# Optimization experiments

Hardware: AMD Instinct MI355X
Metric: run time of the kernel (lower is better)

Reference implementation:

```python
import jax, jax.numpy as jnp
import numpy as np

SEQ_LEN = 4096
EMBED = 1024
HIDDEN = 128
BATCH = 8


def setup_inputs() -> dict:
    key = jax.random.key(0)
    k_in, k_q, k_k, k_v = jax.random.split(key, 4)
    inputs = jax.random.normal(k_in, (BATCH, SEQ_LEN, EMBED), dtype=jnp.float32)
    # nn.Linear(embed, hidden, bias=False) weights; stored [hidden, embed] in torch,
    # we keep [embed, hidden] for x @ W.
    scale = 1.0 / np.sqrt(EMBED)
    Wq = jax.random.uniform(k_q, (EMBED, HIDDEN), jnp.float32, -scale, scale)
    Wk = jax.random.uniform(k_k, (EMBED, HIDDEN), jnp.float32, -scale, scale)
    Wv = jax.random.uniform(k_v, (EMBED, HIDDEN), jnp.float32, -scale, scale)
    return {"inputs": inputs, "Wq": Wq, "Wk": Wk, "Wv": Wv}


def reference(inputs, Wq, Wk, Wv):
    # Single-head causal scaled dot-product attention.
    q = jnp.einsum("bse,eh->bsh", inputs, Wq)
    k = jnp.einsum("bse,eh->bsh", inputs, Wk)
    v = jnp.einsum("bse,eh->bsh", inputs, Wv)
    d_k = q.shape[-1]
    q = q / jnp.sqrt(jnp.asarray(d_k, q.dtype))
    scores = jnp.einsum("bqh,bkh->bqk", q, k)  # [B, S, S]
    seq = scores.shape[-1]
    causal = jnp.tril(jnp.ones((seq, seq), dtype=bool))
    scores = jnp.where(causal, scores, jnp.asarray(-jnp.inf, scores.dtype))
    weights = jax.nn.softmax(scores, axis=-1)
    return jnp.einsum("bqk,bkh->bqh", weights, v)
```

## Files before the change

### kernel.cpp

```cpp
#include <hip/hip_runtime.h>
#include <stdint.h>

#define B_ 8
#define S_ 4096
#define E_ 1024
#define H_ 128
#define M_ (B_*S_)

typedef __attribute__((ext_vector_type(8))) short short8;
typedef __attribute__((ext_vector_type(4))) float f32x4;
typedef __attribute__((ext_vector_type(16))) float f32x16;

static constexpr float QSCALE = 0.08838834764831845f;

__device__ __forceinline__ unsigned short f2bf(float f) {
    uint32_t u = __float_as_uint(f);
    u += 0x7fffu + ((u >> 16) & 1u);
    return (unsigned short)(u >> 16);
}

__device__ __forceinline__ uint32_t cvt_pk_bf16(float a, float b) {
    uint32_t r;
    asm("v_cvt_pk_bf16_f32 %0, %1, %2" : "=v"(r) : "v"(a), "v"(b));
    return r;
}

__device__ __forceinline__ void gl16(const void* g, void* s) {
    __builtin_amdgcn_global_load_lds(
        (const __attribute__((address_space(1))) unsigned int*)g,
        (__attribute__((address_space(3))) unsigned int*)s, 16, 0, 0);
}

__global__ __launch_bounds__(256)
void prep_w_kernel(const float* __restrict__ Wq, const float* __restrict__ Wk,
                   const float* __restrict__ Wv, unsigned short* __restrict__ Wt)
{
    int id = blockIdx.x*256 + threadIdx.x;
    int which = id >> 14;
    int rem = id & 16383;
    int h = rem >> 7, kc = rem & 127;
    const float* __restrict__ W = (which==0)?Wq:((which==1)?Wk:Wv);
    const float scale = (which==0)? QSCALE : 1.0f;
    uint32_t u[4];
    #pragma unroll
    for (int p=0;p<4;++p) {
        unsigned short a = f2bf(W[(size_t)(kc*8 + 2*p  )*H_ + h] * scale);
        unsigned short b = f2bf(W[(size_t)(kc*8 + 2*p+1)*H_ + h] * scale);
        u[p] = (uint32_t)a | ((uint32_t)b << 16);
    }
    uint4 v; v.x=u[0]; v.y=u[1]; v.z=u[2]; v.w=u[3];
    *(uint4*)(Wt + (size_t)(which*H_ + h)*E_ + kc*8) = v;
}

__global__ __launch_bounds__(512)
void proj_kernel(const float* __restrict__ x, const unsigned short* __restrict__ Wt,
                 unsigned short* __restrict__ Qg, unsigned short* __restrict__ Kg,
                 unsigned short* __restrict__ Vtg)
{
    const int t = threadIdx.x;
    const int w = t >> 6, l = t & 63;
    const int grp = l >> 4, li = l & 15;
    const int rg = w & 3, cg = w >> 2;
    const int rb = blockIdx.x;
    const int row0 = rb * 128;

    __shared__ __align__(128) unsigned char smem[65536];
    unsigned char* sX = smem;
    unsigned char* sW = smem + 16384;
    unsigned short* epi = (unsigned short*)smem;

    f32x4 acc[2][12];
    const f32x4 zz = {0.f,0.f,0.f,0.f};
    #pragma unroll
    for (int mt=0;mt<2;++mt)
        #pragma unroll
        for (int nt=0;nt<12;++nt) acc[mt][nt] = zz;

    for (int k0=0; k0<E_; k0+=64) {
        __syncthreads();
        #pragma unroll
        for (int i=0;i<4;++i) {
            int idx = i*512 + t;
            int row = idx >> 4, c4 = idx & 15;
            float4 v = *(const float4*)(x + (size_t)(row0+row)*E_ + k0 + c4*4);
            uint2 pv;
            pv.x = cvt_pk_bf16(v.x, v.y);
            pv.y = cvt_pk_bf16(v.z, v.w);
            *(uint2*)(sX + row*128 + ((c4*8) ^ ((row&7)<<4))) = pv;
        }
        #pragma unroll
        for (int i=0;i<6;++i) {
            int idx = i*512 + t;
            int wr = idx >> 3, cb = (idx & 7) * 16;
            uint4 v = *(const uint4*)((const unsigned char*)Wt + (size_t)wr*2048 + k0*2 + cb);
            *(uint4*)(sW + wr*128 + (cb ^ ((wr&7)<<4))) = v;
        }
        __syncthreads();

        #pragma unroll
        for (int ks=0;ks<2;++ks) {
            short8 af[2];
            #pragma unroll
            for (int mt=0;mt<2;++mt) {
                int row = rg*32 + mt*16 + li;
                af[mt] = *(const short8*)(sX + row*128 + ((ks*64 + grp*16) ^ ((row&7)<<4)));
            }
            #pragma unroll
            for (int nt=0;nt<12;++nt) {
                int wr = cg*192 + nt*16 + li;
                short8 bf = *(const short8*)(sW + wr*128 + ((ks*64 + grp*16) ^ ((wr&7)<<4)));
                #pragma unroll
                for (int mt=0;mt<2;++mt)
                    acc[mt][nt] = __builtin_amdgcn_mfma_f32_16x16x32_bf16(af[mt], bf, acc[mt][nt], 0,0,0);
            }
        }
    }

    const int bidx = rb >> 5;
    const int srow = (rb & 31) * 128;

    __syncthreads();

    if (cg == 0) {
        #pragma unroll
        for (int mt=0;mt<2;++mt)
            #pragma unroll
            for (int nt=0;nt<12;++nt)
                #pragma unroll
                for (int r=0;r<4;++r) {
                    int rowl = rg*32 + mt*16 + grp*4 + r;
                    int col  = nt*16 + li;
                    epi[rowl*208 + col] = f2bf(acc[mt][nt][r]);
                }
    }
    __syncthreads();
    #pragma unroll
    for (int i=0;i<4;++i) {
        int idx = i*512 + t;
        int row = idx >> 4, cc = idx & 15;
        uint4 v = *(const uint4*)((const unsigned char*)epi + row*416 + cc*16);
        *(uint4*)((unsigned char*)Qg + (size_t)(row0+row)*256 + cc*16) = v;
    }
    #pragma unroll
    for (int i=0;i<2;++i) {
        int idx = i*512 + t;
        int row = idx >> 3, cc = idx & 7;
        uint4 v = *(const uint4*)((const unsigned char*)epi + row*416 + 256 + cc*16);
        *(uint4*)((unsigned char*)Kg + (size_t)(row0+row)*256 + cc*16) = v;
    }
    __syncthreads();

    if (cg == 1) {
        #pragma unroll
        for (int mt=0;mt<2;++mt)
            #pragma unroll
            for (int nt=0;nt<12;++nt)
                #pragma unroll
                for (int r=0;r<4;++r) {
                    int rowl = rg*32 + mt*16 + grp*4 + r;
                    int col  = nt*16 + li;
                    epi[rowl*208 + col] = f2bf(acc[mt][nt][r]);
                }
    }
    __syncthreads();
    #pragma unroll
    for (int i=0;i<2;++i) {
        int idx = i*512 + t;
        int row = idx >> 3, cc = idx & 7;
        uint4 v = *(const uint4*)((const unsigned char*)epi + row*416 + cc*16);
        *(uint4*)((unsigned char*)Kg + (size_t)(row0+row)*256 + 128 + cc*16) = v;
    }
    #pragma unroll
    for (int i=0;i<4;++i) {
        int idx = i*512 + t;
        int h = idx >> 4, sc = idx & 15;
        uint32_t u[4];
        #pragma unroll
        for (int p=0;p<4;++p) {
            unsigned short a = epi[(sc*8 + 2*p    )*208 + 64 + h];
            unsigned short b = epi[(sc*8 + 2*p + 1)*208 + 64 + h];
            u[p] = (uint32_t)a | ((uint32_t)b << 16);
        }
        uint4 v; v.x=u[0]; v.y=u[1]; v.z=u[2]; v.w=u[3];
        *(uint4*)(Vtg + (size_t)(bidx*H_ + h)*S_ + srow + sc*8) = v;
    }
}

__device__ __forceinline__ void stage_tile(unsigned char* buf,
                                           const unsigned char* Kb,
                                           const unsigned char* Vb,
                                           int kt, int w, int l)
{
    unsigned char* sVb = buf + 16384;
    #pragma unroll
    for (int j=0;j<2;++j) {
        int A = w*2048 + j*1024 + (l<<4);
        int krow = A >> 8;
        int kin  = A & 255;
        gl16(Kb + (size_t)kt*16384 + krow*256 + (kin ^ ((krow&7)<<4)),
             buf + w*2048 + j*1024);
        int h   = A >> 7;
        int vin = A & 127;
        gl16(Vb + (size_t)h*8192 + (size_t)kt*128 + (vin ^ ((h&7)<<4)),
             sVb + w*2048 + j*1024);
    }
}

__global__ __launch_bounds__(512, 2)
void attn_p1(const unsigned short* __restrict__ Qg,
             const unsigned short* __restrict__ Kg,
             const unsigned short* __restrict__ Vtg,
             float* __restrict__ Pp, float* __restrict__ Ml)
{
    const int t    = threadIdx.x;
    const int w    = t >> 6;
    const int l    = t & 63;
    const int hi   = l >> 5;
    const int c31  = l & 31;
    const int gid  = blockIdx.x;
    const int b    = gid & 7;
    const int rr   = gid >> 3;
    const int c4   = rr & 3;
    const int pr   = rr >> 2;

    __shared__ __align__(128) unsigned char smem[65536];

    const size_t bbase = (size_t)b * S_ * H_;
    const unsigned char* Kb = (const unsigned char*)(Kg + bbase);
    const unsigned char* Vb = (const unsigned char*)(Vtg + (size_t)b*H_*S_);
    const int swzq = (c31 & 7) << 4;

    int cur = 0;
    for (int ph = 0; ph < 2; ++ph) {
        const int qt   = ph ? (15 - pr) : pr;
        const int q0   = qt * 256;
        const int qw0  = q0 + w*32;
        const int qrow = qw0 + c31;
        const int nkt  = 4*(qt+1);

        short8 qf[8];
        {
            const unsigned short* qp = Qg + bbase + (size_t)qrow * H_;
            #pragma unroll
            for (int ks=0; ks<8; ++ks)
                qf[ks] = *(const short8*)(qp + ks*16 + hi*8);
        }

        f32x16 oacc[4];
        #pragma unroll
        for (int ht=0; ht<4; ++ht)
            #pragma unroll
            for (int r=0; r<16; ++r) oacc[ht][r] = 0.f;
        float mrun = -1e30f, lrun = 0.f;

        stage_tile(smem + cur*32768, Kb, Vb, c4, w, l);
        __syncthreads();

        for (int kt = c4; kt < nkt; kt += 4) {
            const bool pre = (kt+4 < nkt);
            if (pre) stage_tile(smem + (cur^1)*32768, Kb, Vb, kt+4, w, l);

            if (kt*64 <= qw0 + 31) {
                const unsigned char* sK = smem + cur*32768;
                const unsigned char* sV = sK + 16384;

                f32x16 sacc[2];
                #pragma unroll
                for (int st=0; st<2; ++st)
                    #pragma unroll
                    for (int r=0; r<16; ++r) sacc[st][r] = 0.f;
                #pragma unroll
                for (int st=0; st<2; ++st) {
                    int krow = st*32 + c31;
                    #pragma unroll
                    for (int ks=0; ks<8; ++ks) {
                        short8 kf = *(const short8*)(sK + krow*256 + ((ks*32 + hi*16) ^ swzq));
                        sacc[st] = __builtin_amdgcn_mfma_f32_32x32x16_bf16(kf, qf[ks], sacc[st], 0,0,0);
                    }
                }

                if (kt*64 + 63 > qw0) {
                    #pragma unroll
                    for (int st=0; st<2; ++st)
                        #pragma unroll
                        for (int r=0; r<16; ++r) {
                            int key = kt*64 + st*32 + (r&3) + 8*(r>>2) + 4*hi;
                            if (key > qrow) sacc[st][r] = -1e30f;
                        }
                }

                float pmax = -1e30f;
                #pragma unroll
                for (int st=0; st<2; ++st)
                    #pragma unroll
                    for (int r=0; r<16; ++r) pmax = fmaxf(pmax, sacc[st][r]);
                pmax = fmaxf(pmax, __shfl_xor(pmax, 32, 64));

                if (!__all(pmax - mrun <= 8.0f)) {
                    float mnew = fmaxf(mrun, pmax);
                    float alpha = __expf(mrun - mnew);
                    #pragma unroll
                    for (int ht=0; ht<4; ++ht)
                        #pragma unroll
                        for (int r=0; r<16; ++r) oacc[ht][r] *= alpha;
                    lrun *= alpha;
                    mrun = mnew;
                }

                float p[2][16];
                float psum = 0.f;
                #pragma unroll
                for (int st=0; st<2; ++st)
                    #pragma unroll
                    for (int r=0; r<16; ++r) {
                        float e = __expf(sacc[st][r] - mrun);
                        p[st][r] = e;
                        psum += e;
                    }
                psum += __shfl_xor(psum, 32, 64);
                lrun += psum;

                short8 pf[4];
                #pragma unroll
                for (int st=0; st<2; ++st) {
                    uint32_t A0 = cvt_pk_bf16(p[st][0],  p[st][1]);
                    uint32_t A1 = cvt_pk_bf16(p[st][2],  p[st][3]);
                    uint32_t B0 = cvt_pk_bf16(p[st][4],  p[st][5]);
                    uint32_t B1 = cvt_pk_bf16(p[st][6],  p[st][7]);
                    uint32_t C0 = cvt_pk_bf16(p[st][8],  p[st][9]);
                    uint32_t C1 = cvt_pk_bf16(p[st][10], p[st][11]);
                    uint32_t D0 = cvt_pk_bf16(p[st][12], p[st][13]);
                    uint32_t D1 = cvt_pk_bf16(p[st][14], p[st][15]);
                    {
                        uint32_t x0 = hi ? A0 : B0;
                        uint32_t x1 = hi ? A1 : B1;
                        uint32_t y0 = (uint32_t)__shfl_xor((int)x0, 32, 64);
                        uint32_t y1 = (uint32_t)__shfl_xor((int)x1, 32, 64);
                        union { uint32_t u[4]; short8 s; } uu;
                        uu.u[0] = hi ? y0 : A0;
                        uu.u[1] = hi ? y1 : A1;
                        uu.u[2] = hi ? B0 : y0;
                        uu.u[3] = hi ? B1 : y1;
                        pf[st*2] = uu.s;
                    }
                    {
                        uint32_t x0 = hi ? C0 : D0;
                        uint32_t x1 = hi ? C1 : D1;
                        uint32_t y0 = (uint32_t)__shfl_xor((int)x0, 32, 64);
                        uint32_t y1 = (uint32_t)__shfl_xor((int)x1, 32, 64);
                        union { uint32_t u[4]; short8 s; } uu;
                        uu.u[0] = hi ? y0 : C0;
                        uu.u[1] = hi ? y1 : C1;
                        uu.u[2] = hi ? D0 : y0;
                        uu.u[3] = hi ? D1 : y1;
                        pf[st*2+1] = uu.s;
                    }
                }

                #pragma unroll
                for (int sl=0; sl<4; ++sl) {
                    #pragma unroll
                    for (int ht=0; ht<4; ++ht) {
                        int h = ht*32 + c31;
                        short8 vf = *(const short8*)(sV + h*128 + ((sl*32 + hi*16) ^ swzq));
                        oacc[ht] = __builtin_amdgcn_mfma_f32_32x32x16_bf16(vf, pf[sl], oacc[ht], 0,0,0);
                    }
                }
            }

            __syncthreads();
            if (pre) cur ^= 1;
        }

        float* Prow = Pp + (size_t)c4*((size_t)M_*H_) + bbase + (size_t)qrow*H_;
        #pragma unroll
        for (int ht=0; ht<4; ++ht)
            #pragma unroll
            for (int k=0; k<4; ++k) {
                float4 o;
                o.x = oacc[ht][4*k+0];
                o.y = oacc[ht][4*k+1];
                o.z = oacc[ht][4*k+2];
                o.w = oacc[ht][4*k+3];
                *(float4*)(Prow + ht*32 + 8*k + 4*hi) = o;
            }
        if (hi == 0) {
            float2 ml2; ml2.x = mrun; ml2.y = lrun;
            *(float2*)(Ml + ((size_t)c4*M_ + (size_t)b*S_ + qrow)*2) = ml2;
        }
    }
}

__global__ __launch_bounds__(256)
void attn_merge(const float* __restrict__ Pp, const float* __restrict__ Ml,
                float* __restrict__ Out)
{
    int gid = blockIdx.x*256 + threadIdx.x;
    int q  = gid >> 5;
    int h4 = gid & 31;

    float m0 = Ml[((size_t)0*M_ + q)*2], l0 = Ml[((size_t)0*M_ + q)*2 + 1];
    float m1 = Ml[((size_t)1*M_ + q)*2], l1 = Ml[((size_t)1*M_ + q)*2 + 1];
    float m2 = Ml[((size_t)2*M_ + q)*2], l2 = Ml[((size_t)2*M_ + q)*2 + 1];
    float m3 = Ml[((size_t)3*M_ + q)*2], l3 = Ml[((size_t)3*M_ + q)*2 + 1];

    float M = fmaxf(fmaxf(m0, m1), fmaxf(m2, m3));
    float w0 = __expf(m0 - M), w1 = __expf(m1 - M);
    float w2 = __expf(m2 - M), w3 = __expf(m3 - M);
    float L = w0*l0 + w1*l1 + w2*l2 + w3*l3;

    float4 p0 = *(const float4*)(Pp + (size_t)0*((size_t)M_*H_) + (size_t)q*H_ + h4*4);
    float4 p1 = *(const float4*)(Pp + (size_t)1*((size_t)M_*H_) + (size_t)q*H_ + h4*4);
    float4 p2 = *(const float4*)(Pp + (size_t)2*((size_t)M_*H_) + (size_t)q*H_ + h4*4);
    float4 p3 = *(const float4*)(Pp + (size_t)3*((size_t)M_*H_) + (size_t)q*H_ + h4*4);
    float inv = 1.0f / L;
    float4 o;
    o.x = (w0*p0.x + w1*p1.x + w2*p2.x + w3*p3.x) * inv;
    o.y = (w0*p0.y + w1*p1.y + w2*p2.y + w3*p3.y) * inv;
    o.z = (w0*p0.z + w1*p1.z + w2*p2.z + w3*p3.z) * inv;
    o.w = (w0*p0.w + w1*p1.w + w2*p2.w + w3*p3.w) * inv;
    *(float4*)(Out + (size_t)q*H_ + h4*4) = o;
}

__global__ __launch_bounds__(128, 1)
void attn_fb(const unsigned short* __restrict__ Qg,
             const unsigned short* __restrict__ Kg,
             const unsigned short* __restrict__ Vtg,
             float* __restrict__ Out)
{
    const int t   = threadIdx.x;
    const int w   = t >> 6;
    const int l   = t & 63;
    const int hi  = l >> 5;
    const int c31 = l & 31;
    const int qt  = (S_/64 - 1) - blockIdx.x;
    const int b   = blockIdx.y;
    const int q0  = qt * 64;
    const int qrow = q0 + w*32 + c31;

    __shared__ __align__(128) unsigned char sK[16384];
    __shared__ __align__(128) unsigned char sV[16384];

    const size_t bbase = (size_t)b * S_ * H_;

    short8 qf[8];
    {
        const unsigned short* qp = Qg + bbase + (size_t)qrow * H_;
        #pragma unroll
        for (int ks=0; ks<8; ++ks)
            qf[ks] = *(const short8*)(qp + ks*16 + hi*8);
    }

    f32x16 oacc[4];
    #pragma unroll
    for (int ht=0; ht<4; ++ht)
        #pragma unroll
        for (int r=0; r<16; ++r) oacc[ht][r] = 0.f;
    float mrun = -1e30f, lrun = 0.f;

    const unsigned char* Kb = (const unsigned char*)(Kg + bbase);
    const unsigned char* Vb = (const unsigned char*)(Vtg + (size_t)b*H_*S_);
    const int swzq = (c31 & 7) << 4;

    for (int kt=0; kt<=qt; ++kt) {
        __syncthreads();
        #pragma unroll
        for (int i=0;i<8;++i) {
            int c = i*128 + t;
            int row = c >> 4, cb = (c & 15) * 16;
            *(uint4*)(sK + row*256 + (cb ^ ((row&7)<<4))) =
                *(const uint4*)(Kb + (size_t)(kt*64 + row)*256 + cb);
        }
        #pragma unroll
        for (int i=0;i<8;++i) {
            int c = i*128 + t;
            int h = c >> 3, cb = (c & 7) * 16;
            *(uint4*)(sV + h*128 + (cb ^ ((h&7)<<4))) =
                *(const uint4*)(Vb + (size_t)h*(S_*2) + kt*128 + cb);
        }
        __syncthreads();

        f32x16 sacc[2];
        #pragma unroll
        for (int st=0; st<2; ++st)
            #pragma unroll
            for (int r=0; r<16; ++r) sacc[st][r] = 0.f;
        #pragma unroll
        for (int st=0; st<2; ++st) {
            int krow = st*32 + c31;
            #pragma unroll
            for (int ks=0; ks<8; ++ks) {
                short8 kf = *(const short8*)(sK + krow*256 + ((ks*32 + hi*16) ^ swzq));
                sacc[st] = __builtin_amdgcn_mfma_f32_32x32x16_bf16(kf, qf[ks], sacc[st], 0,0,0);
            }
        }

        if (kt == qt) {
            #pragma unroll
            for (int st=0; st<2; ++st)
                #pragma unroll
                for (int r=0; r<16; ++r) {
                    int key = q0 + st*32 + (r&3) + 8*(r>>2) + 4*hi;
                    if (key > qrow) sacc[st][r] = -1e30f;
                }
        }

        float pmax = -1e30f;
        #pragma unroll
        for (int st=0; st<2; ++st)
            #pragma unroll
            for (int r=0; r<16; ++r) pmax = fmaxf(pmax, sacc[st][r]);
        pmax = fmaxf(pmax, __shfl_xor(pmax, 32, 64));

        if (!__all(pmax - mrun <= 8.0f)) {
            float mnew = fmaxf(mrun, pmax);
            float alpha = __expf(mrun - mnew);
            #pragma unroll
            for (int ht=0; ht<4; ++ht)
                #pragma unroll
                for (int r=0; r<16; ++r) oacc[ht][r] *= alpha;
            lrun *= alpha;
            mrun = mnew;
        }

        float p[2][16];
        float psum = 0.f;
        #pragma unroll
        for (int st=0; st<2; ++st)
            #pragma unroll
            for (int r=0; r<16; ++r) {
                float e = __expf(sacc[st][r] - mrun);
                p[st][r] = e;
                psum += e;
            }
        psum += __shfl_xor(psum, 32, 64);
        lrun += psum;

        short8 pf[4];
        #pragma unroll
        for (int st=0; st<2; ++st) {
            uint32_t A0 = cvt_pk_bf16(p[st][0],  p[st][1]);
            uint32_t A1 = cvt_pk_bf16(p[st][2],  p[st][3]);
            uint32_t B0 = cvt_pk_bf16(p[st][4],  p[st][5]);
            uint32_t B1 = cvt_pk_bf16(p[st][6],  p[st][7]);
            uint32_t C0 = cvt_pk_bf16(p[st][8],  p[st][9]);
            uint32_t C1 = cvt_pk_bf16(p[st][10], p[st][11]);
            uint32_t D0 = cvt_pk_bf16(p[st][12], p[st][13]);
            uint32_t D1 = cvt_pk_bf16(p[st][14], p[st][15]);
            {
                uint32_t x0 = hi ? A0 : B0;
                uint32_t x1 = hi ? A1 : B1;
                uint32_t y0 = (uint32_t)__shfl_xor((int)x0, 32, 64);
                uint32_t y1 = (uint32_t)__shfl_xor((int)x1, 32, 64);
                union { uint32_t u[4]; short8 s; } uu;
                uu.u[0] = hi ? y0 : A0;
                uu.u[1] = hi ? y1 : A1;
                uu.u[2] = hi ? B0 : y0;
                uu.u[3] = hi ? B1 : y1;
                pf[st*2] = uu.s;
            }
            {
                uint32_t x0 = hi ? C0 : D0;
                uint32_t x1 = hi ? C1 : D1;
                uint32_t y0 = (uint32_t)__shfl_xor((int)x0, 32, 64);
                uint32_t y1 = (uint32_t)__shfl_xor((int)x1, 32, 64);
                union { uint32_t u[4]; short8 s; } uu;
                uu.u[0] = hi ? y0 : C0;
                uu.u[1] = hi ? y1 : C1;
                uu.u[2] = hi ? D0 : y0;
                uu.u[3] = hi ? D1 : y1;
                pf[st*2+1] = uu.s;
            }
        }

        #pragma unroll
        for (int sl=0; sl<4; ++sl) {
            #pragma unroll
            for (int ht=0; ht<4; ++ht) {
                int h = ht*32 + c31;
                short8 vf = *(const short8*)(sV + h*128 + ((sl*32 + hi*16) ^ swzq));
                oacc[ht] = __builtin_amdgcn_mfma_f32_32x32x16_bf16(vf, pf[sl], oacc[ht], 0,0,0);
            }
        }
    }

    float linv = 1.0f / lrun;
    float* Op = Out + bbase + (size_t)qrow * H_;
    #pragma unroll
    for (int ht=0; ht<4; ++ht)
        #pragma unroll
        for (int k=0; k<4; ++k) {
            float4 o;
            o.x = oacc[ht][4*k+0] * linv;
            o.y = oacc[ht][4*k+1] * linv;
            o.z = oacc[ht][4*k+2] * linv;
            o.w = oacc[ht][4*k+3] * linv;
            *(float4*)(Op + ht*32 + 8*k + 4*hi) = o;
        }
}

extern "C" void kernel_launch(void* const* d_in, const int* in_sizes, int n_in,
                              void* d_out, int out_size, void* d_ws, size_t ws_size,
                              hipStream_t stream) {
    const float* x  = (const float*)d_in[0];
    const float* Wq = (const float*)d_in[1];
    const float* Wk = (const float*)d_in[2];
    const float* Wv = (const float*)d_in[3];

    unsigned char* ws = (unsigned char*)d_ws;
    unsigned short* Wt  = (unsigned short*)ws;
    unsigned short* Qg  = (unsigned short*)(ws + 1048576u);
    unsigned short* Kg  = (unsigned short*)(ws + 9437184u);
    unsigned short* Vtg = (unsigned short*)(ws + 17825792u);
    float* Pp = (float*)(ws + 26214400u);
    float* Ml = (float*)(ws + 93323264u);
    const size_t NEED = 94371840u;

    prep_w_kernel<<<192, 256, 0, stream>>>(Wq, Wk, Wv, Wt);
    proj_kernel<<<256, 512, 0, stream>>>(x, Wt, Qg, Kg, Vtg);

    if (ws_size >= NEED) {
        attn_p1<<<256, 512, 0, stream>>>(Qg, Kg, Vtg, Pp, Ml);
        attn_merge<<<4096, 256, 0, stream>>>(Pp, Ml, (float*)d_out);
    } else {
        dim3 ga(S_/64, B_);
        attn_fb<<<ga, 128, 0, stream>>>(Qg, Kg, Vtg, (float*)d_out);
    }
}
```

Baseline: 120.8 us.

## Double-buffer projection GEMM with direct global-to-LDS loads and in-register bf16 conversion

The projection kernel now stages raw fp32 x tiles and pre-swizzled bf16 W tiles into LDS using direct global-to-LDS loads (gl16) into two ping-pong buffers. The next K-slice is prefetched while the current one is consumed, and each loop iteration has one barrier instead of two. The fp32-to-bf16 conversion of x moves from the staging path to the fragment read. The W prep kernel writes a new swizzled layout that matches the LDS layout. In exchange the kernel uses more LDS (80KB), which may reduce occupancy, and reads twice as many LDS bytes for the x operand.

Measured after the change: 125.7 us. 1.04x slower.

```diff
diff --git a/kernel.cpp b/kernel.cpp
--- a/kernel.cpp
+++ b/kernel.cpp
@@ -49,7 +49,28 @@
         u[p] = (uint32_t)a | ((uint32_t)b << 16);
     }
     uint4 v; v.x=u[0]; v.y=u[1]; v.z=u[2]; v.w=u[3];
-    *(uint4*)(Wt + (size_t)(which*H_ + h)*E_ + kc*8) = v;
+    int gp = (kc >> 2)*64 + (((kc & 3)*16) ^ ((h & 3) << 4));
+    *(uint4*)((unsigned char*)Wt + (size_t)(which*H_ + h)*2048 + gp) = v;
+}
+
+__device__ __forceinline__ void proj_stage(unsigned char* buf,
+                                           const unsigned char* xb,
+                                           const unsigned char* Wb,
+                                           int i, int w, int l)
+{
+    #pragma unroll
+    for (int j=0;j<5;++j) {
+        int cb = w*5120 + j*1024;
+        int A  = cb + (l << 4);
+        if (cb < 16384) {
+            int row = A >> 7, col = A & 127;
+            gl16(xb + (size_t)row*4096 + i*128 + (col ^ ((row & 7) << 4)), buf + cb);
+        } else {
+            int A2 = A - 16384;
+            int wr = A2 >> 6, w6 = A2 & 63;
+            gl16(Wb + (size_t)wr*2048 + i*64 + w6, buf + 16384 + (cb - 16384));
+        }
+    }
 }
 
 __global__ __launch_bounds__(512)
@@ -64,10 +85,11 @@
     const int rb = blockIdx.x;
     const int row0 = rb * 128;
 
-    __shared__ __align__(128) unsigned char smem[65536];
-    unsigned char* sX = smem;
-    unsigned char* sW = smem + 16384;
+    __shared__ __align__(128) unsigned char smem[81920];
     unsigned short* epi = (unsigned short*)smem;
+
+    const unsigned char* xb = (const unsigned char*)x + (size_t)row0*4096;
+    const unsigned char* Wb = (const unsigned char*)Wt;
 
     f32x4 acc[2][12];
     const f32x4 zz = {0.f,0.f,0.f,0.f};
@@ -76,50 +98,44 @@
         #pragma unroll
         for (int nt=0;nt<12;++nt) acc[mt][nt] = zz;
 
-    for (int k0=0; k0<E_; k0+=64) {
+    proj_stage(smem, xb, Wb, 0, w, l);
+    __syncthreads();
+
+    int cur = 0;
+    for (int i=0; i<32; ++i) {
+        if (i+1 < 32) proj_stage(smem + (cur^1)*40960, xb, Wb, i+1, w, l);
+
+        const unsigned char* sX = smem + cur*40960;
+        const unsigned char* sW = sX + 16384;
+
+        short8 af[2];
+        #pragma unroll
+        for (int mt=0;mt<2;++mt) {
+            int row = rg*32 + mt*16 + li;
+            int sw = (row & 7) << 4;
+            float4 a0 = *(const float4*)(sX + row*128 + ((grp*32     ) ^ sw));
+            float4 a1 = *(const float4*)(sX + row*128 + ((grp*32 + 16) ^ sw));
+            union { uint32_t u[4]; short8 s; } pa;
+            pa.u[0] = cvt_pk_bf16(a0.x, a0.y);
+            pa.u[1] = cvt_pk_bf16(a0.z, a0.w);
+            pa.u[2] = cvt_pk_bf16(a1.x, a1.y);
+            pa.u[3] = cvt_pk_bf16(a1.z, a1.w);
+            af[mt] = pa.s;
+        }
+        #pragma unroll
+        for (int nt=0;nt<12;++nt) {
+            int wr = cg*192 + nt*16 + li;
+            short8 bf = *(const short8*)(sW + wr*64 + ((grp*16) ^ ((wr & 3) << 4)));
+            acc[0][nt] = __builtin_amdgcn_mfma_f32_16x16x32_bf16(af[0], bf, acc[0][nt], 0,0,0);
+            acc[1][nt] = __builtin_amdgcn_mfma_f32_16x16x32_bf16(af[1], bf, acc[1][nt], 0,0,0);
+        }
+
         __syncthreads();
-        #pragma unroll
-        for (int i=0;i<4;++i) {
-            int idx = i*512 + t;
-            int row = idx >> 4, c4 = idx & 15;
-            float4 v = *(const float4*)(x + (size_t)(row0+row)*E_ + k0 + c4*4);
-            uint2 pv;
-            pv.x = cvt_pk_bf16(v.x, v.y);
-            pv.y = cvt_pk_bf16(v.z, v.w);
-            *(uint2*)(sX + row*128 + ((c4*8) ^ ((row&7)<<4))) = pv;
-        }
-        #pragma unroll
-        for (int i=0;i<6;++i) {
-            int idx = i*512 + t;
-            int wr = idx >> 3, cb = (idx & 7) * 16;
-            uint4 v = *(const uint4*)((const unsigned char*)Wt + (size_t)wr*2048 + k0*2 + cb);
-            *(uint4*)(sW + wr*128 + (cb ^ ((wr&7)<<4))) = v;
-        }
-        __syncthreads();
-
-        #pragma unroll
-        for (int ks=0;ks<2;++ks) {
-            short8 af[2];
-            #pragma unroll
-            for (int mt=0;mt<2;++mt) {
-                int row = rg*32 + mt*16 + li;
-                af[mt] = *(const short8*)(sX + row*128 + ((ks*64 + grp*16) ^ ((row&7)<<4)));
-            }
-            #pragma unroll
-            for (int nt=0;nt<12;++nt) {
-                int wr = cg*192 + nt*16 + li;
-                short8 bf = *(const short8*)(sW + wr*128 + ((ks*64 + grp*16) ^ ((wr&7)<<4)));
-                #pragma unroll
-                for (int mt=0;mt<2;++mt)
-                    acc[mt][nt] = __builtin_amdgcn_mfma_f32_16x16x32_bf16(af[mt], bf, acc[mt][nt], 0,0,0);
-            }
-        }
+        cur ^= 1;
     }
 
     const int bidx = rb >> 5;
     const int srow = (rb & 31) * 128;
-
-    __syncthreads();
 
     if (cg == 0) {
         #pragma unroll
```
